# Optimization experiments

Measured on AMD Instinct MI355X. Metric: run time of the kernel, lower is better.

## Reference

```python
import jax, jax.numpy as jnp
import numpy as np

NEG_INF = -1e30


def _cc_attention(q, k, v):
    # q,k: [B,H,W,c], v: [B,H,W,C]
    B, H, W, _ = q.shape
    # vertical scores over column: [B,H,W,H], diag (h==g) masked out
    sv = jnp.einsum('bhwc,bgwc->bhwg', q, k)
    eye = jnp.eye(H, dtype=bool)[:, None, :]  # [H,1,H]
    sv = jnp.where(eye, NEG_INF, sv)
    # horizontal scores over row: [B,H,W,W]
    sh = jnp.einsum('bhwc,bhuc->bhwu', q, k)
    a = jax.nn.softmax(jnp.concatenate([sv, sh], axis=-1), axis=-1)
    av, ah = a[..., :H], a[..., H:H + W]
    yv = jnp.einsum('bhwg,bgwc->bhwc', av, v)
    yh = jnp.einsum('bhwu,bhuc->bhwc', ah, v)
    return yv + yh


def setup_inputs() -> dict:
    key = jax.random.key(0)
    ks = jax.random.split(key, 7)
    B, H, W, C = 8, 96, 96, 512
    c = C // 8
    s = lambda n: 1.0 / np.sqrt(n)
    return {
        'x': jax.random.normal(ks[0], (B, H, W, C), jnp.float32),
        'Wq': jax.random.normal(ks[1], (C, c), jnp.float32) * s(C),
        'bq': jnp.zeros((c,), jnp.float32),
        'Wk': jax.random.normal(ks[2], (C, c), jnp.float32) * s(C),
        'bk': jnp.zeros((c,), jnp.float32),
        'Wv': jax.random.normal(ks[3], (C, C), jnp.float32) * s(C),
        'bv': jnp.zeros((C,), jnp.float32),
        'gamma': jnp.float32(0.5),
    }


def reference(x, Wq, bq, Wk, bk, Wv, bv, gamma):
    # 1x1 convs == per-pixel matmul
    q = jnp.einsum('bhwc,cd->bhwd', x, Wq) + bq
    k = jnp.einsum('bhwc,cd->bhwd', x, Wk) + bk
    v = jnp.einsum('bhwc,cd->bhwd', x, Wv) + bv
    y = _cc_attention(q, k, v) * gamma
    return y + x
```

## Files before the change

kernel.cpp:

```cpp
#include <hip/hip_runtime.h>
#include <hip/hip_bf16.h>


#define NPIX 73728
#define CC 512
#define CQ 64
#define PA 384

typedef __attribute__((ext_vector_type(8))) short bf16x8;
typedef __attribute__((ext_vector_type(4))) float f32x4;

__device__ __forceinline__ short bf16s(float f) {
    __hip_bfloat16 h = __float2bfloat16(f);
    return *reinterpret_cast<short*>(&h);
}

__device__ __forceinline__ float bf2f(short s) {
    return __uint_as_float(((unsigned int)(unsigned short)s) << 16);
}

__global__ __launch_bounds__(256) void conv_w(
    const float* __restrict__ W, short* __restrict__ dst, int J)
{
    int idx = blockIdx.x * 256 + threadIdx.x;
    int lane = idx & 63;
    int blk = idx >> 6;
    int ntiles = J >> 4;
    int ntile = blk % ntiles;
    int kb32 = blk / ntiles;
    int krow = kb32 * 32 + (lane >> 4) * 8;
    int col = ntile * 16 + (lane & 15);
    union { short h[8]; uint4 u; } pk;
    #pragma unroll
    for (int j = 0; j < 8; ++j)
        pk.h[j] = bf16s(W[(size_t)(krow + j) * J + col]);
    *reinterpret_cast<uint4*>(dst + (size_t)idx * 8) = pk.u;
}

__global__ __launch_bounds__(256) void proj_qk(
    const float* __restrict__ x,
    const short* __restrict__ Wqf, const short* __restrict__ Wkf,
    const float* __restrict__ bq, const float* __restrict__ bk,
    short* __restrict__ q, short* __restrict__ k)
{
    __shared__ __align__(16) short Sbuf[128 * 136];
    const int tid = threadIdx.x;
    const int lane = tid & 63;
    const int w = tid >> 6;
    const int mBase = blockIdx.x * 128;
    const int wr = w >> 1;
    const int wsel = w & 1;
    const short* Wf = wsel ? Wkf : Wqf;
    const float* bias = wsel ? bk : bq;

    f32x4 acc[4][4];
    #pragma unroll
    for (int i = 0; i < 4; ++i)
        #pragma unroll
        for (int j = 0; j < 4; ++j) {
            f32x4 z = {0.f, 0.f, 0.f, 0.f};
            acc[i][j] = z;
        }

    for (int kb = 0; kb < 16; ++kb) {
        #pragma unroll
        for (int s = 0; s < 2; ++s) {
            int seg = tid + 256 * s;
            int r = seg >> 2, kq = seg & 3;
            const float* src = x + (size_t)(mBase + r) * 512 + kb * 32 + kq * 8;
            float4 f0 = *reinterpret_cast<const float4*>(src);
            float4 f1 = *reinterpret_cast<const float4*>(src + 4);
            union { short h[8]; bf16x8 v; } pk;
            pk.h[0] = bf16s(f0.x); pk.h[1] = bf16s(f0.y);
            pk.h[2] = bf16s(f0.z); pk.h[3] = bf16s(f0.w);
            pk.h[4] = bf16s(f1.x); pk.h[5] = bf16s(f1.y);
            pk.h[6] = bf16s(f1.z); pk.h[7] = bf16s(f1.w);
            int dlane = (r & 15) + 16 * kq;
            *reinterpret_cast<bf16x8*>(&Sbuf[(r >> 4) * 512 + dlane * 8]) = pk.v;
        }
        __syncthreads();

        bf16x8 bf[4], af[4];
        #pragma unroll
        for (int jn = 0; jn < 4; ++jn)
            bf[jn] = *reinterpret_cast<const bf16x8*>(
                Wf + ((size_t)(kb * 4 + jn) * 64 + lane) * 8);
        #pragma unroll
        for (int i = 0; i < 4; ++i)
            af[i] = *reinterpret_cast<const bf16x8*>(&Sbuf[(wr * 4 + i) * 512 + lane * 8]);
        #pragma unroll
        for (int i = 0; i < 4; ++i)
            #pragma unroll
            for (int jn = 0; jn < 4; ++jn)
                acc[i][jn] = __builtin_amdgcn_mfma_f32_16x16x32_bf16(
                    af[i], bf[jn], acc[i][jn], 0, 0, 0);
        __syncthreads();
    }

    const int lrow = (lane >> 4) * 4, cl = lane & 15;
    #pragma unroll
    for (int jn = 0; jn < 4; ++jn) {
        float bc = bias[jn * 16 + cl];
        #pragma unroll
        for (int i = 0; i < 4; ++i) {
            int row = wr * 64 + i * 16 + lrow;
            #pragma unroll
            for (int r = 0; r < 4; ++r)
                Sbuf[(row + r) * 136 + wsel * 64 + jn * 16 + cl] =
                    bf16s(acc[i][jn][r] + bc);
        }
    }
    __syncthreads();
    #pragma unroll
    for (int i = 0; i < 8; ++i) {
        int id = tid + 256 * i;
        int arr = id >> 10;
        int rem = id & 1023;
        int pix = rem >> 3, cc = rem & 7;
        bf16x8 vv = *reinterpret_cast<const bf16x8*>(&Sbuf[pix * 136 + arr * 64 + cc * 8]);
        short* dst = arr ? k : q;
        *reinterpret_cast<bf16x8*>(dst + (size_t)(mBase + pix) * 64 + cc * 8) = vv;
    }
}

__global__ __launch_bounds__(256) void proj_v(
    const float* __restrict__ x, const short* __restrict__ Wvf,
    const float* __restrict__ bv, short* __restrict__ vth)
{
    __shared__ __align__(16) short Albuf[128 * 32];
    const int tid = threadIdx.x;
    const int lane = tid & 63;
    const int w = tid >> 6;
    const int bid = blockIdx.x;
    const int mBase = (bid >> 2) * 128;
    const int nBase = (bid & 3) * 128;

    const int wr = w >> 1, wc = w & 1;
    const int nTile0 = (nBase >> 4) + wc * 4;

    f32x4 acc[4][4];
    #pragma unroll
    for (int i = 0; i < 4; ++i)
        #pragma unroll
        for (int j = 0; j < 4; ++j) {
            f32x4 z = {0.f, 0.f, 0.f, 0.f};
            acc[i][j] = z;
        }

    for (int kb = 0; kb < 16; ++kb) {
        #pragma unroll
        for (int s = 0; s < 2; ++s) {
            int seg = tid + 256 * s;
            int r = seg >> 2, kq = seg & 3;
            const float* src = x + (size_t)(mBase + r) * 512 + kb * 32 + kq * 8;
            float4 f0 = *reinterpret_cast<const float4*>(src);
            float4 f1 = *reinterpret_cast<const float4*>(src + 4);
            union { short h[8]; bf16x8 v; } pk;
            pk.h[0] = bf16s(f0.x); pk.h[1] = bf16s(f0.y);
            pk.h[2] = bf16s(f0.z); pk.h[3] = bf16s(f0.w);
            pk.h[4] = bf16s(f1.x); pk.h[5] = bf16s(f1.y);
            pk.h[6] = bf16s(f1.z); pk.h[7] = bf16s(f1.w);
            int dlane = (r & 15) + 16 * kq;
            *reinterpret_cast<bf16x8*>(&Albuf[(r >> 4) * 512 + dlane * 8]) = pk.v;
        }
        __syncthreads();

        bf16x8 bf[4], af[4];
        #pragma unroll
        for (int jn = 0; jn < 4; ++jn)
            bf[jn] = *reinterpret_cast<const bf16x8*>(
                Wvf + ((size_t)(kb * 32 + nTile0 + jn) * 64 + lane) * 8);
        #pragma unroll
        for (int i = 0; i < 4; ++i)
            af[i] = *reinterpret_cast<const bf16x8*>(&Albuf[(wr * 4 + i) * 512 + lane * 8]);
        #pragma unroll
        for (int i = 0; i < 4; ++i)
            #pragma unroll
            for (int jn = 0; jn < 4; ++jn)
                acc[i][jn] = __builtin_amdgcn_mfma_f32_16x16x32_bf16(
                    af[i], bf[jn], acc[i][jn], 0, 0, 0);
        __syncthreads();
    }

    const int lrow = (lane >> 4) * 4, lcol = lane & 15;
    #pragma unroll
    for (int jn = 0; jn < 4; ++jn) {
        int col = nBase + wc * 64 + jn * 16 + lcol;
        float bc = bv[col];
        #pragma unroll
        for (int i = 0; i < 4; ++i) {
            int row = mBase + wr * 64 + i * 16 + lrow;
            short4 st;
            st.x = bf16s(acc[i][jn][0] + bc);
            st.y = bf16s(acc[i][jn][1] + bc);
            st.z = bf16s(acc[i][jn][2] + bc);
            st.w = bf16s(acc[i][jn][3] + bc);
            *reinterpret_cast<short4*>(vth + (size_t)col * NPIX + row) = st;
        }
    }
}

__global__ __launch_bounds__(256) void transpose_vtv(
    const short* __restrict__ vth, short* __restrict__ vtv)
{
    __shared__ short T[96 * 97];
    const int tid = threadIdx.x;
    const size_t plane = (size_t)blockIdx.x * 9216;
    const short* src = vth + plane;
    short* dst = vtv + plane;

    for (int id = tid; id < 1152; id += 256) {
        int h = id / 12, w8 = (id % 12) * 8;
        bf16x8 v = *reinterpret_cast<const bf16x8*>(src + h * 96 + w8);
        #pragma unroll
        for (int j = 0; j < 8; ++j) T[h * 97 + w8 + j] = v[j];
    }
    __syncthreads();
    for (int id = tid; id < 1152; id += 256) {
        int ww = id / 12, h8 = (id % 12) * 8;
        union { short h[8]; bf16x8 v; } pk;
        #pragma unroll
        for (int j = 0; j < 8; ++j) pk.h[j] = T[(h8 + j) * 97 + ww];
        *reinterpret_cast<bf16x8*>(dst + ww * 96 + h8) = pk.v;
    }
}

__global__ __launch_bounds__(256) void cc_scores(
    const short* __restrict__ Q,
    const short* __restrict__ K,
    float* __restrict__ S)
{
    __shared__ __align__(16) float Ss[96 * 100];
    const int tid = threadIdx.x;
    const int lane = tid & 63;
    const int wv = tid >> 6;
    const int wr = wv >> 1, wc = wv & 1;
    const bool vert = (blockIdx.y == 0);
    const int b = blockIdx.x / 96;
    const int line = blockIdx.x % 96;

    size_t base;
    int rowStride;
    if (vert) { base = (size_t)b * 9216 + line;       rowStride = 96; }
    else      { base = ((size_t)b * 96 + line) * 96;  rowStride = 1;  }

    const int cl = lane & 15;
    const int q8 = (lane >> 4) * 8;

    f32x4 acc[3][3];
    #pragma unroll
    for (int i = 0; i < 3; ++i)
        #pragma unroll
        for (int j = 0; j < 3; ++j) {
            f32x4 z = {0.f, 0.f, 0.f, 0.f};
            acc[i][j] = z;
        }

    #pragma unroll
    for (int kb = 0; kb < 2; ++kb) {
        bf16x8 af[3], bf[3];
        #pragma unroll
        for (int mt = 0; mt < 3; ++mt) {
            size_t n = base + (size_t)(wr * 48 + mt * 16 + cl) * rowStride;
            af[mt] = *reinterpret_cast<const bf16x8*>(Q + n * 64 + kb * 32 + q8);
        }
        #pragma unroll
        for (int nt = 0; nt < 3; ++nt) {
            size_t n = base + (size_t)(wc * 48 + nt * 16 + cl) * rowStride;
            bf[nt] = *reinterpret_cast<const bf16x8*>(K + n * 64 + kb * 32 + q8);
        }
        #pragma unroll
        for (int mt = 0; mt < 3; ++mt)
            #pragma unroll
            for (int nt = 0; nt < 3; ++nt)
                acc[mt][nt] = __builtin_amdgcn_mfma_f32_16x16x32_bf16(
                    af[mt], bf[nt], acc[mt][nt], 0, 0, 0);
    }

    const int lrow = (lane >> 4) * 4;
    #pragma unroll
    for (int mt = 0; mt < 3; ++mt) {
        #pragma unroll
        for (int r = 0; r < 4; ++r) {
            int i = wr * 48 + mt * 16 + lrow + r;
            #pragma unroll
            for (int nt = 0; nt < 3; ++nt) {
                int j = wc * 48 + nt * 16 + cl;
                Ss[i * 100 + j] = (vert && i == j) ? -1e30f : acc[mt][nt][r];
            }
        }
    }
    __syncthreads();

    const int dirOff = vert ? 0 : 96;
    #pragma unroll
    for (int t = 0; t < 9; ++t) {
        int id = tid + 256 * t;
        int i = id / 24, j4 = (id % 24) * 4;
        f32x4 v = *reinterpret_cast<const f32x4*>(&Ss[i * 100 + j4]);
        size_t n = base + (size_t)i * rowStride;
        *reinterpret_cast<f32x4*>(S + n * 192 + dirOff + j4) = v;
    }
}

__global__ __launch_bounds__(256) void cc_softmax(float* __restrict__ S)
{
    const int tid = threadIdx.x;
    const int lane = tid & 63;
    const size_t n = (size_t)blockIdx.x * 4 + (tid >> 6);
    float* row = S + n * 192;
    float s0 = row[lane], s1 = row[lane + 64], s2 = row[lane + 128];
    float m = fmaxf(s0, fmaxf(s1, s2));
    #pragma unroll
    for (int off = 32; off >= 1; off >>= 1) m = fmaxf(m, __shfl_xor(m, off, 64));
    float e0 = expf(s0 - m), e1 = expf(s1 - m), e2 = expf(s2 - m);
    float sum = e0 + e1 + e2;
    #pragma unroll
    for (int off = 32; off >= 1; off >>= 1) sum += __shfl_xor(sum, off, 64);
    float inv = 1.0f / sum;
    short p0 = bf16s(e0 * inv);
    short p1 = bf16s(e1 * inv);
    short p2 = bf16s(e2 * inv);
    short* av = reinterpret_cast<short*>(row);
    short* ah = av + 96;
    av[lane] = p0;
    if (lane < 32) av[64 + lane] = p1;
    else           ah[lane - 32] = p1;
    ah[32 + lane] = p2;
}

__global__ __launch_bounds__(256) void cc_aggr_v(
    const short* __restrict__ A,
    const short* __restrict__ vtv,
    short* __restrict__ Yv)
{
    __shared__ __align__(16) short Yb[96 * 136];
    const int tid = threadIdx.x;
    const int lane = tid & 63;
    const int wv = tid >> 6;
    const int bid = blockIdx.x;
    const int pair = bid >> 2;
    const int cBase = (bid & 3) * 128;
    const int b = pair / 96;
    const int w = pair - b * 96;
    const size_t pixBase = (size_t)b * 9216 + w;
    const size_t wBase = (size_t)b * 9216 + (size_t)w * 96;

    const int wr = wv >> 1, wc = wv & 1;
    const int cl = lane & 15, q = lane >> 4;

    f32x4 acc[3][4];
    #pragma unroll
    for (int i = 0; i < 3; ++i)
        #pragma unroll
        for (int j = 0; j < 4; ++j) {
            f32x4 z = {0.f, 0.f, 0.f, 0.f};
            acc[i][j] = z;
        }

    #pragma unroll
    for (int kb = 0; kb < 3; ++kb) {
        bf16x8 af[3];
        #pragma unroll
        for (int mt = 0; mt < 3; ++mt) {
            size_t n = pixBase + (size_t)(wr * 48 + mt * 16 + cl) * 96;
            af[mt] = *reinterpret_cast<const bf16x8*>(A + n * PA + kb * 32 + q * 8);
        }
        #pragma unroll
        for (int nt = 0; nt < 4; ++nt) {
            int col = cBase + wc * 64 + nt * 16 + cl;
            bf16x8 bv = *reinterpret_cast<const bf16x8*>(
                vtv + (size_t)col * NPIX + wBase + kb * 32 + q * 8);
            #pragma unroll
            for (int mt = 0; mt < 3; ++mt)
                acc[mt][nt] = __builtin_amdgcn_mfma_f32_16x16x32_bf16(
                    af[mt], bv, acc[mt][nt], 0, 0, 0);
        }
    }

    const int lrow = q * 4;
    #pragma unroll
    for (int mt = 0; mt < 3; ++mt) {
        #pragma unroll
        for (int r = 0; r < 4; ++r) {
            int hl = wr * 48 + mt * 16 + lrow + r;
            #pragma unroll
            for (int nt = 0; nt < 4; ++nt)
                Yb[hl * 136 + wc * 64 + nt * 16 + cl] = bf16s(acc[mt][nt][r]);
        }
    }
    __syncthreads();
    #pragma unroll
    for (int i = 0; i < 6; ++i) {
        int id = tid + 256 * i;
        int hh = id >> 4, cc = id & 15;
        bf16x8 v = *reinterpret_cast<const bf16x8*>(&Yb[hh * 136 + cc * 8]);
        *reinterpret_cast<bf16x8*>(
            Yv + (pixBase + (size_t)hh * 96) * 512 + cBase + cc * 8) = v;
    }
}

__global__ __launch_bounds__(256) void cc_aggr_h_final(
    const short* __restrict__ A,
    const short* __restrict__ vth,
    const short* __restrict__ Yv,
    const float* __restrict__ X,
    const float* __restrict__ gamma_p,
    float* __restrict__ out)
{
    __shared__ __align__(16) float Yh[96 * 132];
    const int tid = threadIdx.x;
    const int lane = tid & 63;
    const int wv = tid >> 6;
    const int bid = blockIdx.x;
    const int pair = bid >> 2;
    const int cBase = (bid & 3) * 128;
    const size_t rowBase = (size_t)pair * 96;

    const int wr = wv >> 1, wc = wv & 1;
    const int cl = lane & 15, q = lane >> 4;

    f32x4 acc[3][4];
    #pragma unroll
    for (int i = 0; i < 3; ++i)
        #pragma unroll
        for (int j = 0; j < 4; ++j) {
            f32x4 z = {0.f, 0.f, 0.f, 0.f};
            acc[i][j] = z;
        }

    #pragma unroll
    for (int kb = 0; kb < 3; ++kb) {
        bf16x8 af[3];
        #pragma unroll
        for (int mt = 0; mt < 3; ++mt) {
            size_t n = rowBase + (size_t)(wr * 48 + mt * 16 + cl);
            af[mt] = *reinterpret_cast<const bf16x8*>(A + n * PA + 96 + kb * 32 + q * 8);
        }
        #pragma unroll
        for (int nt = 0; nt < 4; ++nt) {
            int col = cBase + wc * 64 + nt * 16 + cl;
            bf16x8 bv = *reinterpret_cast<const bf16x8*>(
                vth + (size_t)col * NPIX + rowBase + kb * 32 + q * 8);
            #pragma unroll
            for (int mt = 0; mt < 3; ++mt)
                acc[mt][nt] = __builtin_amdgcn_mfma_f32_16x16x32_bf16(
                    af[mt], bv, acc[mt][nt], 0, 0, 0);
        }
    }

    const int lrow = q * 4;
    #pragma unroll
    for (int mt = 0; mt < 3; ++mt) {
        #pragma unroll
        for (int r = 0; r < 4; ++r) {
            int wl = wr * 48 + mt * 16 + lrow + r;
            #pragma unroll
            for (int nt = 0; nt < 4; ++nt)
                Yh[wl * 132 + wc * 64 + nt * 16 + cl] = acc[mt][nt][r];
        }
    }
    __syncthreads();

    const float gm = gamma_p[0];
    #pragma unroll
    for (int i = 0; i < 12; ++i) {
        int id = tid + 256 * i;
        int rw = id >> 5, c4 = (id & 31) * 4;
        f32x4 yh = *reinterpret_cast<const f32x4*>(&Yh[rw * 132 + c4]);
        size_t off = (rowBase + rw) * 512 + cBase + c4;
        float4 xx = *reinterpret_cast<const float4*>(X + off);
        short4 yv = *reinterpret_cast<const short4*>(Yv + off);
        float4 o;
        o.x = (yh[0] + bf2f(yv.x)) * gm + xx.x;
        o.y = (yh[1] + bf2f(yv.y)) * gm + xx.y;
        o.z = (yh[2] + bf2f(yv.z)) * gm + xx.z;
        o.w = (yh[3] + bf2f(yv.w)) * gm + xx.w;
        *reinterpret_cast<float4*>(out + off) = o;
    }
}

extern "C" void kernel_launch(void* const* d_in, const int* in_sizes, int n_in,
                              void* d_out, int out_size, void* d_ws, size_t ws_size,
                              hipStream_t stream) {
    const float* x     = (const float*)d_in[0];
    const float* Wq    = (const float*)d_in[1];
    const float* bq    = (const float*)d_in[2];
    const float* Wk    = (const float*)d_in[3];
    const float* bk    = (const float*)d_in[4];
    const float* Wv    = (const float*)d_in[5];
    const float* bv    = (const float*)d_in[6];
    const float* gamma = (const float*)d_in[7];
    float* out = (float*)d_out;

    short* Wqf = (short*)d_ws;
    short* Wkf = Wqf + 512 * 64;
    short* Wvf = Wkf + 512 * 64;
    short* q   = Wvf + 512 * 512;
    short* k   = q + (size_t)NPIX * CQ;
    short* vth = k + (size_t)NPIX * CQ;
    short* vtv = vth + (size_t)NPIX * CC;
    short* Yv  = vtv + (size_t)NPIX * CC;
    float* S   = (float*)(Yv + (size_t)NPIX * CC);

    conv_w<<<16, 256, 0, stream>>>(Wq, Wqf, 64);
    conv_w<<<16, 256, 0, stream>>>(Wk, Wkf, 64);
    conv_w<<<128, 256, 0, stream>>>(Wv, Wvf, 512);

    proj_qk<<<NPIX / 128, 256, 0, stream>>>(x, Wqf, Wkf, bq, bk, q, k);
    proj_v<<<(NPIX / 128) * 4, 256, 0, stream>>>(x, Wvf, bv, vth);
    transpose_vtv<<<4096, 256, 0, stream>>>(vth, vtv);

    cc_scores<<<dim3(8 * 96, 2), 256, 0, stream>>>(q, k, S);
    cc_softmax<<<NPIX / 4, 256, 0, stream>>>(S);

    cc_aggr_v<<<768 * 4, 256, 0, stream>>>((const short*)S, vtv, Yv);
    cc_aggr_h_final<<<768 * 4, 256, 0, stream>>>(
        (const short*)S, vth, Yv, x, gamma, out);
}
```

Measured before the change: 582.1 us.

## Merge weight conversion launches, remap x staging loads, and XCD-swizzle proj_v blocks

Combines the three weight-conversion kernels into one launch to cut launch overhead. Reorders the x-staging thread mapping in proj_qk and proj_v so each thread writes LDS contiguously at G*8, with the global reads now arranged by MFMA fragment lane. Remaps proj_v block indices so the four N-slabs of the same M-tile land on the same XCD, aiming to improve L2 reuse of x. The new global access pattern has consecutive threads reading different rows, which may reduce coalescing.

```diff
diff --git a/kernel.cpp b/kernel.cpp
--- a/kernel.cpp
+++ b/kernel.cpp
@@ -19,10 +19,17 @@
     return __uint_as_float(((unsigned int)(unsigned short)s) << 16);
 }
 
-__global__ __launch_bounds__(256) void conv_w(
-    const float* __restrict__ W, short* __restrict__ dst, int J)
-{
-    int idx = blockIdx.x * 256 + threadIdx.x;
+__global__ __launch_bounds__(256) void conv_w3(
+    const float* __restrict__ Wq, const float* __restrict__ Wk,
+    const float* __restrict__ Wv,
+    short* __restrict__ Wqf, short* __restrict__ Wkf, short* __restrict__ Wvf)
+{
+    int bid = blockIdx.x;
+    const float* W; short* dst; int J; int base;
+    if (bid < 16)      { W = Wq; dst = Wqf; J = 64;  base = 0;  }
+    else if (bid < 32) { W = Wk; dst = Wkf; J = 64;  base = 16; }
+    else               { W = Wv; dst = Wvf; J = 512; base = 32; }
+    int idx = (bid - base) * 256 + threadIdx.x;
     int lane = idx & 63;
     int blk = idx >> 6;
     int ntiles = J >> 4;
@@ -65,9 +72,10 @@
     for (int kb = 0; kb < 16; ++kb) {
         #pragma unroll
         for (int s = 0; s < 2; ++s) {
-            int seg = tid + 256 * s;
-            int r = seg >> 2, kq = seg & 3;
-            const float* src = x + (size_t)(mBase + r) * 512 + kb * 32 + kq * 8;
+            int G = tid + 256 * s;
+            int dl = G & 63;
+            int row = ((G >> 6) << 4) + (dl & 15);
+            const float* src = x + (size_t)(mBase + row) * 512 + kb * 32 + (dl >> 4) * 8;
             float4 f0 = *reinterpret_cast<const float4*>(src);
             float4 f1 = *reinterpret_cast<const float4*>(src + 4);
             union { short h[8]; bf16x8 v; } pk;
@@ -75,8 +83,7 @@
             pk.h[2] = bf16s(f0.z); pk.h[3] = bf16s(f0.w);
             pk.h[4] = bf16s(f1.x); pk.h[5] = bf16s(f1.y);
             pk.h[6] = bf16s(f1.z); pk.h[7] = bf16s(f1.w);
-            int dlane = (r & 15) + 16 * kq;
-            *reinterpret_cast<bf16x8*>(&Sbuf[(r >> 4) * 512 + dlane * 8]) = pk.v;
+            *reinterpret_cast<bf16x8*>(&Sbuf[G * 8]) = pk.v;
         }
         __syncthreads();
 
@@ -132,8 +139,12 @@
     const int lane = tid & 63;
     const int w = tid >> 6;
     const int bid = blockIdx.x;
-    const int mBase = (bid >> 2) * 128;
-    const int nBase = (bid & 3) * 128;
+    const int xcd = bid & 7;
+    const int jj = bid >> 3;
+    const int slab = jj & 3;
+    const int g = (jj >> 2) * 8 + xcd;
+    const int mBase = g * 128;
+    const int nBase = slab * 128;
 
     const int wr = w >> 1, wc = w & 1;
     const int nTile0 = (nBase >> 4) + wc * 4;
@@ -150,9 +161,10 @@
     for (int kb = 0; kb < 16; ++kb) {
         #pragma unroll
         for (int s = 0; s < 2; ++s) {
-            int seg = tid + 256 * s;
-            int r = seg >> 2, kq = seg & 3;
-            const float* src = x + (size_t)(mBase + r) * 512 + kb * 32 + kq * 8;
+            int G = tid + 256 * s;
+            int dl = G & 63;
+            int row = ((G >> 6) << 4) + (dl & 15);
+            const float* src = x + (size_t)(mBase + row) * 512 + kb * 32 + (dl >> 4) * 8;
             float4 f0 = *reinterpret_cast<const float4*>(src);
             float4 f1 = *reinterpret_cast<const float4*>(src + 4);
             union { short h[8]; bf16x8 v; } pk;
@@ -160,8 +172,7 @@
             pk.h[2] = bf16s(f0.z); pk.h[3] = bf16s(f0.w);
             pk.h[4] = bf16s(f1.x); pk.h[5] = bf16s(f1.y);
             pk.h[6] = bf16s(f1.z); pk.h[7] = bf16s(f1.w);
-            int dlane = (r & 15) + 16 * kq;
-            *reinterpret_cast<bf16x8*>(&Albuf[(r >> 4) * 512 + dlane * 8]) = pk.v;
+            *reinterpret_cast<bf16x8*>(&Albuf[G * 8]) = pk.v;
         }
         __syncthreads();
 
@@ -503,9 +514,7 @@
     short* Yv  = vtv + (size_t)NPIX * CC;
     float* S   = (float*)(Yv + (size_t)NPIX * CC);
 
-    conv_w<<<16, 256, 0, stream>>>(Wq, Wqf, 64);
-    conv_w<<<16, 256, 0, stream>>>(Wk, Wkf, 64);
-    conv_w<<<128, 256, 0, stream>>>(Wv, Wvf, 512);
+    conv_w3<<<160, 256, 0, stream>>>(Wq, Wk, Wv, Wqf, Wkf, Wvf);
 
     proj_qk<<<NPIX / 128, 256, 0, stream>>>(x, Wqf, Wkf, bq, bk, q, k);
     proj_v<<<(NPIX / 128) * 4, 256, 0, stream>>>(x, Wvf, bv, vth);
```

Measured after the change: 584.8 us. About the same (+0.5%).
